# Kernel tuning notes

Hardware: AMD Instinct MI355X
Metric: run time of the kernel (lower is better)

Reference implementation:

```python
import jax, jax.numpy as jnp
import numpy as np

# Config matching init_kwargs
DILS = [1, 3, 6, 12]          # flattened dilations for blocks [[1,3],[6,12]]
BLOCK_START = [0, 2]          # layer index where each block starts
IN = 64                       # input_size
SS = 256                      # state_size
HS = 128                      # h_size
OS = SS - HS                  # out_size for S2Cell
OUT = 8                       # output_size
B = 1024                      # batch (number of series)
T = 256                       # timesteps
# per-layer lxh input widths: [in, out, out+in, out] each + 2*h
IN_SIZES = [IN + 2 * HS, OS + 2 * HS, OS + IN + 2 * HS, OS + 2 * HS]


def setup_inputs() -> dict:
    key = jax.random.key(0)
    ks = jax.random.split(key, 12)
    d = {"x": jax.random.normal(ks[0], (T, B, IN), jnp.float32)}
    for i in range(4):
        fan_in = IN_SIZES[i]
        d[f"W{i}"] = jax.random.normal(ks[1 + i], (4 * SS, fan_in), jnp.float32) / np.sqrt(fan_in)
        d[f"b{i}"] = jnp.zeros((4 * SS,), jnp.float32)
    d["Wout"] = jax.random.normal(ks[9], (OUT, OS), jnp.float32) / np.sqrt(OS)
    d["bout"] = jnp.zeros((OUT,), jnp.float32)
    return d


def _s2cell(t, inp, W, b, prevH, prevC, bufH, bufC, dil):
    """One S2Cell step. bufH/bufC are circular buffers of length dil holding
    states from the last `dil` steps; bufH[t % dil] is the state from t-dil."""
    idx = t % dil
    has_del = t >= dil
    dH = jnp.where(has_del, bufH[idx], prevH)   # [B, HS]
    dC = bufC[idx]                               # [B, SS] (only used when has_del)
    xh = jnp.concatenate([inp, prevH, dH], axis=1)
    gates = xh @ W.T + b                         # [B, 4*SS]
    g0, g1, g2, g3 = jnp.split(gates, 4, axis=1)
    forget = jax.nn.sigmoid(g0 + 1.0)
    cand = jnp.tanh(g1)
    alpha = jax.nn.sigmoid(g2)
    out_gate = jax.nn.sigmoid(g3)
    weightedC = jnp.where(has_del, alpha * prevC + (1.0 - alpha) * dC, prevC)
    newC = jnp.where(t >= 1, forget * weightedC + (1.0 - forget) * cand, cand)
    whole = out_gate * newC                      # [B, SS]
    out_t, h = whole[:, :OS], whole[:, OS:]
    return out_t, h, newC, bufH.at[idx].set(h), bufC.at[idx].set(newC)


def reference(x, W0, b0, W1, b1, W2, b2, W3, b3, Wout, bout):
    Ws = [W0, W1, W2, W3]
    bs = [b0, b1, b2, b3]

    def init_layer(d):
        return (jnp.zeros((B, HS), x.dtype), jnp.zeros((B, SS), x.dtype),
                jnp.zeros((d, B, HS), x.dtype), jnp.zeros((d, B, SS), x.dtype))

    carry0 = (jnp.int32(0), tuple(init_layer(d) for d in DILS))

    def step(carry, x_t):
        t, states = carry
        new_states = []
        inp = x_t
        for li in range(4):
            if li in BLOCK_START and li > 0:
                # first layer of a later block: cat(previous block output, original input)
                inp = jnp.concatenate([inp, x_t], axis=1)
            prevH, prevC, bufH, bufC = states[li]
            inp, h, c, bufH, bufC = _s2cell(t, inp, Ws[li], bs[li], prevH, prevC, bufH, bufC, DILS[li])
            new_states.append((h, c, bufH, bufC))
        y = inp @ Wout.T + bout
        return (t + 1, tuple(new_states)), y

    _, ys = jax.lax.scan(step, carry0, x)
    return ys  # [T, B, OUT]
```

## Files before the change

### kernel.cpp

```cpp
#include <hip/hip_runtime.h>
#include <stdint.h>
#include <stdio.h>


typedef __attribute__((ext_vector_type(8))) short short8;
typedef __attribute__((ext_vector_type(4))) float f32x4;

#define DEVINL static __device__ __forceinline__

constexpr int TT = 256, BBATCH = 1024, INW = 64, HSW = 128, OSW = 128, NO = 8;
constexpr int ROWS = 128;

constexpr int KLa[4]   = {192, 384, 448, 384};
constexpr int DILa[4]  = {1, 3, 6, 12};
constexpr int PERa[4]  = {2, 4, 7, 13};
constexpr int WOFFa[4] = {0, 6144, 18432, 32768};
constexpr int WBYTES   = 90112;

constexpr int BIAS_B  = WBYTES;
constexpr int WOUT_B  = BIAS_B + 512;
constexpr int WSTR    = 129;
constexpr int BOUT_B  = WOUT_B + 8 * WSTR * 4;
constexpr int C3_B    = BOUT_B + 32;
constexpr int LDS_BYTES = C3_B + 12 * 256 * 16;

constexpr size_t WSBASE    = 8192;
constexpr size_t BH_OFF[4] = {0, 65536, 196608, 425984};
constexpr size_t OUTB_OFF  = 851968;
constexpr size_t CB_OFF    = 983040;
constexpr size_t C1_SZ     = 32 * 3 * 256 * 16;
constexpr size_t C2_SZ     = 32 * 6 * 256 * 16;
constexpr size_t CLSZ      = CB_OFF + C1_SZ + C2_SZ;
constexpr size_t WS_NEED   = WSBASE + 8 * CLSZ;

__host__ __device__ constexpr int seg_type(int L, int k) {
  if (L == 0) return k < 64 ? 0 : 2;
  if (L == 1) return k < 128 ? 1 : (k < 256 ? 2 : 3);
  if (L == 2) return k < 128 ? 1 : (k < 192 ? 0 : (k < 320 ? 2 : 3));
  return k < 128 ? 1 : (k < 256 ? 2 : 3);
}
__host__ __device__ constexpr int seg_start(int L, int k) {
  if (L == 0) return k < 64 ? 0 : 64;
  if (L == 1) return k < 128 ? 0 : (k < 256 ? 128 : 256);
  if (L == 2) return k < 128 ? 0 : (k < 192 ? 128 : (k < 320 ? 192 : 320));
  return k < 128 ? 0 : (k < 256 ? 128 : 256);
}

template <int N> struct IC { static constexpr int value = N; };

DEVINL unsigned short f2bf(float f) {
  union { float f; uint32_t u; } v; v.f = f;
  return (unsigned short)((v.u + 0x7FFFu + ((v.u >> 16) & 1u)) >> 16);
}
DEVINL float bf2f(unsigned short h) {
  union { uint32_t u; float f; } v; v.u = ((uint32_t)h) << 16;
  return v.f;
}
DEVINL float sigm(float x)  { return 1.0f / (1.0f + __expf(-x)); }
DEVINL float tanh_(float x) { return 1.0f - 2.0f / (__expf(2.0f * x) + 1.0f); }

DEVINL short8 zero_s8() { short8 v; for (int i = 0; i < 8; i++) v[i] = 0; return v; }
DEVINL f32x4  zero_f4() { f32x4  v; for (int i = 0; i < 4; i++) v[i] = 0.f; return v; }

DEVINL f32x4 mfma16(short8 a, short8 b, f32x4 c) {
  return __builtin_amdgcn_mfma_f32_16x16x32_bf16(a, b, c, 0, 0, 0);
}

DEVINL short8 ld8f(const float* p) {
  const f32x4 u0 = *(const f32x4*)p;
  const f32x4 u1 = *(const f32x4*)(p + 4);
  short8 r;
  r[0] = (short)f2bf(u0[0]); r[1] = (short)f2bf(u0[1]);
  r[2] = (short)f2bf(u0[2]); r[3] = (short)f2bf(u0[3]);
  r[4] = (short)f2bf(u1[0]); r[5] = (short)f2bf(u1[1]);
  r[6] = (short)f2bf(u1[2]); r[7] = (short)f2bf(u1[3]);
  return r;
}

__global__ void __launch_bounds__(256, 1)
rnn_stack_kernel(const float* __restrict__ x,
                 const float* __restrict__ W0, const float* __restrict__ b0,
                 const float* __restrict__ W1, const float* __restrict__ b1,
                 const float* __restrict__ W2, const float* __restrict__ b2,
                 const float* __restrict__ W3, const float* __restrict__ b3,
                 const float* __restrict__ Wout, const float* __restrict__ bout,
                 float* __restrict__ yout, char* __restrict__ ws)
{
  extern __shared__ char smem[];
  unsigned short* wlds = (unsigned short*)smem;
  float* biasl = (float*)(smem + BIAS_B);
  float* woutl = (float*)(smem + WOUT_B);
  float* boutl = (float*)(smem + BOUT_B);
  float* c3l   = (float*)(smem + C3_B);

  const int tid = threadIdx.x;

  __shared__ unsigned s_cg;
  if (tid == 0) {
    unsigned xcc;
    asm volatile("s_getreg_b32 %0, hwreg(HW_REG_XCC_ID)" : "=s"(xcc));
    xcc &= 7u;
    unsigned rank = __hip_atomic_fetch_add(
        (unsigned*)(ws + 4096 + (size_t)xcc * 64), 1u,
        __ATOMIC_RELAXED, __HIP_MEMORY_SCOPE_AGENT);
    s_cg = (xcc << 8) | (rank & 31u);
  }
  __syncthreads();
  const int c = __builtin_amdgcn_readfirstlane((int)(s_cg >> 8));
  const int g = __builtin_amdgcn_readfirstlane((int)(s_cg & 255));

  char* cb = ws + WSBASE + (size_t)c * CLSZ;
  unsigned short* bufH[4];
  unsigned short* outb[4];
#pragma unroll
  for (int l = 0; l < 4; l++) {
    bufH[l] = (unsigned short*)(cb + BH_OFF[l]);
    outb[l] = (unsigned short*)(cb + OUTB_OFF + (size_t)l * ROWS * OSW * 2);
  }
  float* bufC1 = (float*)(cb + CB_OFF + (size_t)g * (3 * 256 * 16));
  float* bufC2 = (float*)(cb + CB_OFF + C1_SZ + (size_t)g * (6 * 256 * 16));

  {
    const float* Wsrc[4] = {W0, W1, W2, W3};
    const float* bsrc[4] = {b0, b1, b2, b3};
    for (int l = 0; l < 4; l++) {
      const int K = KLa[l];
      const int Ksrc = (l == 0) ? 320 : K;
      unsigned short* base = wlds + WOFFa[l];
      for (int n = 0; n < 32; n++) {
        const int grow = (n >> 3) * 256 + g * 8 + (n & 7);
        const float* src = Wsrc[l] + (size_t)grow * Ksrc;
        for (int k = tid; k < K; k += 256) {
          float v = src[k];
          if (l == 0 && k >= 64) v += src[k + 128];
          base[((k >> 5) * 2 + (n >> 4)) * 512 + (n & 15) * 32 +
               ((k >> 3) & 3) * 8 + (k & 7)] = f2bf(v);
        }
      }
      if (tid < 32) biasl[l * 32 + tid] = bsrc[l][(tid >> 3) * 256 + g * 8 + (tid & 7)];
    }
    for (int i = tid; i < 8 * 128; i += 256) woutl[(i >> 7) * WSTR + (i & 127)] = Wout[i];
    if (tid < 8) boutl[tid] = bout[tid];
  }
  __syncthreads();

  const int wv = tid >> 6, lane = tid & 63, lm = lane & 15, quad = lane >> 4;
  const int m0 = wv * 32;
  const bool hi = lm >= 8;
  const int j = lm & 7;
  const int mrow = m0 + (hi ? 16 : 0) + quad * 4;

  unsigned* flg = (unsigned*)(ws + (size_t)c * 512 + (size_t)wv * 128);

  f32x4 pc[4];
#pragma unroll
  for (int l = 0; l < 4; l++) pc[l] = zero_f4();

  f32x4 dc1 = zero_f4(), dc2 = zero_f4(), dc3 = zero_f4();

  auto arrive = [&](unsigned ep) {
    asm volatile("s_waitcnt vmcnt(0)" ::: "memory");
    if (lane == 0)
      __hip_atomic_store(flg + g, ep, __ATOMIC_RELAXED, __HIP_MEMORY_SCOPE_AGENT);
  };
  auto waitbar = [&](unsigned ep) {
    asm volatile("" ::: "memory");
    for (;;) {
      unsigned v = __hip_atomic_load(flg + (lane & 31), __ATOMIC_RELAXED,
                                     __HIP_MEMORY_SCOPE_AGENT);
      if (__all((int)(v >= ep))) break;
    }
    asm volatile("buffer_inv sc0" ::: "memory");
  };

  auto cellpub = [&](auto Lc, int t, f32x4& A00, f32x4& A01, f32x4& A10, f32x4& A11) {
    constexpr int L = decltype(Lc)::value;
    constexpr int DL = DILa[L];
    constexpr int P = PERa[L];
    f32x4 s00, s01, s10, s11;
#pragma unroll
    for (int r = 0; r < 4; r++) {
      s00[r] = __shfl_xor(A00[r], 8);
      s01[r] = __shfl_xor(A01[r], 8);
      s10[r] = __shfl_xor(A10[r], 8);
      s11[r] = __shfl_xor(A11[r], 8);
    }
    f32x4 G0, G1, G2, G3;
#pragma unroll
    for (int r = 0; r < 4; r++) {
      G0[r] = hi ? s10[r] : A00[r];
      G1[r] = hi ? A10[r] : s00[r];
      G2[r] = hi ? s11[r] : A01[r];
      G3[r] = hi ? A11[r] : s01[r];
    }
    const f32x4 pcv = pc[L];
    f32x4 dC = zero_f4();
    if constexpr (L == 1) dC = dc1;
    if constexpr (L == 2) dC = dc2;
    if constexpr (L == 3) dC = dc3;
    f32x4 nC, wh;
#pragma unroll
    for (int q = 0; q < 4; q++) {
      const float fg = sigm(G0[q]);
      const float cd = tanh_(G1[q]);
      const float og = sigm(G3[q]);
      float wc;
      if constexpr (L == 0) {
        wc = pcv[q];
      } else {
        const float al = sigm(G2[q]);
        wc = (t >= DL) ? (al * pcv[q] + (1.0f - al) * dC[q]) : pcv[q];
      }
      const float nc = (t >= 1) ? (fg * wc + (1.0f - fg) * cd) : cd;
      nC[q] = nc;
      wh[q] = og * nc;
    }
    if constexpr (L == 1) *(f32x4*)(bufC1 + ((size_t)(t % 3) * 256 + tid) * 4) = nC;
    if constexpr (L == 2) *(f32x4*)(bufC2 + ((size_t)(t % 6) * 256 + tid) * 4) = nC;
    if constexpr (L == 3) *(f32x4*)(c3l + ((size_t)(t % 12) * 256 + tid) * 4) = nC;
    pc[L] = nC;
    const int jg = g * 8 + j;
#pragma unroll
    for (int r = 0; r < 4; r++) {
      const unsigned short us = f2bf(wh[r]);
      const int row = mrow + r;
      if (g < 16) outb[L][(size_t)row * OSW + jg] = us;
      else bufH[L][((size_t)(t % P) * ROWS + row) * HSW + (jg - 128)] = us;
    }
  };

  auto preL = [&](auto Lc, int t, f32x4& A00, f32x4& A01, f32x4& A10, f32x4& A11) {
    constexpr int L = decltype(Lc)::value;
    constexpr int NKT = KLa[L] / 32;
    constexpr int DL = DILa[L];
    constexpr int P = PERa[L];
    const unsigned short* wl = wlds + WOFFa[L];
    const float bb0 = biasl[L * 32 + lm] + (lm < 8 ? 1.0f : 0.0f);
    const float bb1 = biasl[L * 32 + 16 + lm];
    A00 = (f32x4){bb0, bb0, bb0, bb0};
    A10 = A00;
    A01 = (f32x4){bb1, bb1, bb1, bb1};
    A11 = A01;
    const unsigned short* phb =
        (t >= 1) ? bufH[L] + (size_t)((t - 1) % P) * ROWS * HSW : nullptr;
    const unsigned short* dhb =
        (t >= DL) ? bufH[L] + (size_t)((t - DL) % P) * ROWS * HSW : phb;
    const float* xb = x + ((size_t)t * BBATCH + (size_t)c * ROWS) * INW;
#pragma unroll
    for (int kt = 0; kt < NKT; kt++) {
      const int sty = seg_type(L, kt * 32);
      if (sty == 1) continue;
      const int sst = seg_start(L, kt * 32);
      const int kloc = kt * 32 - sst + quad * 8;
      short8 a0, a1;
      if (sty == 0) {
        const float* p = xb + (size_t)(m0 + lm) * INW + kloc;
        a0 = ld8f(p);
        a1 = ld8f(p + 16 * INW);
      } else {
        const unsigned short* sb = (sty == 2) ? phb : dhb;
        if (sb) {
          const unsigned short* p = sb + (size_t)(m0 + lm) * HSW + kloc;
          a0 = *(const short8*)p;
          a1 = *(const short8*)(p + 16 * HSW);
        } else {
          a0 = zero_s8();
          a1 = zero_s8();
        }
      }
      const short8 bf0v = *(const short8*)(wl + (kt * 2 + 0) * 512 + lm * 32 + quad * 8);
      const short8 bf1v = *(const short8*)(wl + (kt * 2 + 1) * 512 + lm * 32 + quad * 8);
      A00 = mfma16(a0, bf0v, A00);
      A01 = mfma16(a0, bf1v, A01);
      A10 = mfma16(a1, bf0v, A10);
      A11 = mfma16(a1, bf1v, A11);
    }
  };

  auto postL = [&](auto Lc, int t, f32x4& A00, f32x4& A01, f32x4& A10, f32x4& A11) {
    constexpr int L = decltype(Lc)::value;
    const unsigned short* wl = wlds + WOFFa[L];
    const unsigned short* ob = outb[L - 1];
#pragma unroll
    for (int kt = 0; kt < 4; kt++) {
      const int kloc = kt * 32 + quad * 8;
      const unsigned short* p = ob + (size_t)(m0 + lm) * HSW + kloc;
      const short8 a0 = *(const short8*)p;
      const short8 a1 = *(const short8*)(p + 16 * HSW);
      const short8 bf0v = *(const short8*)(wl + (kt * 2 + 0) * 512 + lm * 32 + quad * 8);
      const short8 bf1v = *(const short8*)(wl + (kt * 2 + 1) * 512 + lm * 32 + quad * 8);
      A00 = mfma16(a0, bf0v, A00);
      A01 = mfma16(a0, bf1v, A01);
      A10 = mfma16(a1, bf0v, A10);
      A11 = mfma16(a1, bf1v, A11);
    }
    cellpub(Lc, t, A00, A01, A10, A11);
  };

  auto fullL0 = [&](int t) {
    if (t >= TT) return;
    f32x4 A00, A01, A10, A11;
    const unsigned short* wl = wlds + WOFFa[0];
    const float bb0 = biasl[lm] + (lm < 8 ? 1.0f : 0.0f);
    const float bb1 = biasl[16 + lm];
    A00 = (f32x4){bb0, bb0, bb0, bb0};
    A10 = A00;
    A01 = (f32x4){bb1, bb1, bb1, bb1};
    A11 = A01;
    const unsigned short* phb =
        (t >= 1) ? bufH[0] + (size_t)((t - 1) & 1) * ROWS * HSW : nullptr;
    const float* xb = x + ((size_t)t * BBATCH + (size_t)c * ROWS) * INW;
#pragma unroll
    for (int kt = 0; kt < 6; kt++) {
      const int sty = seg_type(0, kt * 32);
      const int sst = seg_start(0, kt * 32);
      const int kloc = kt * 32 - sst + quad * 8;
      short8 a0, a1;
      if (sty == 0) {
        const float* p = xb + (size_t)(m0 + lm) * INW + kloc;
        a0 = ld8f(p);
        a1 = ld8f(p + 16 * INW);
      } else if (phb) {
        const unsigned short* p = phb + (size_t)(m0 + lm) * HSW + kloc;
        a0 = *(const short8*)p;
        a1 = *(const short8*)(p + 16 * HSW);
      } else {
        a0 = zero_s8();
        a1 = zero_s8();
      }
      const short8 bf0v = *(const short8*)(wl + (kt * 2 + 0) * 512 + lm * 32 + quad * 8);
      const short8 bf1v = *(const short8*)(wl + (kt * 2 + 1) * 512 + lm * 32 + quad * 8);
      A00 = mfma16(a0, bf0v, A00);
      A01 = mfma16(a0, bf1v, A01);
      A10 = mfma16(a1, bf0v, A10);
      A11 = mfma16(a1, bf1v, A11);
    }
    cellpub(IC<0>{}, t, A00, A01, A10, A11);
  };

  auto touchx = [&](int t) {
    if (t >= TT) return;
    const float* xt = x + ((size_t)t * BBATCH + (size_t)c * ROWS + m0) * INW
                      + (size_t)lane * 32;
    float tmp;
    asm volatile("global_load_dword %0, %1, off"
                 : "=v"(tmp) : "v"(xt) : "memory");
  };

  auto epilogue = [&](int tt) {
    if (tt < 0) return;
    const int r = m0 + g;
    const unsigned short* orow = outb[3] + (size_t)r * OSW;
    const int o = lane >> 3, s = lane & 7;
    const short8 v0 = *(const short8*)(orow + s * 16);
    const short8 v1 = *(const short8*)(orow + s * 16 + 8);
    float part = 0.f;
#pragma unroll
    for (int i = 0; i < 8; i++)
      part += bf2f((unsigned short)v0[i]) * woutl[o * WSTR + s * 16 + i];
#pragma unroll
    for (int i = 0; i < 8; i++)
      part += bf2f((unsigned short)v1[i]) * woutl[o * WSTR + s * 16 + 8 + i];
    part += __shfl_down(part, 4);
    part += __shfl_down(part, 2);
    part += __shfl_down(part, 1);
    if (s == 0)
      yout[((size_t)tt * BBATCH + (size_t)c * ROWS + r) * NO + o] = part + boutl[o];
  };

  f32x4 a1_00, a1_01, a1_10, a1_11;
  f32x4 a2_00, a2_01, a2_10, a2_11;
  f32x4 a3_00, a3_01, a3_10, a3_11;

  fullL0(0);
  unsigned ep = 0;
  for (int t = 0; t < TT; t++) {
    if (t > 0) postL3_label: ;
    if (t > 0) postL(IC<3>{}, t - 1, a3_00, a3_01, a3_10, a3_11);
    arrive(++ep);
    preL(IC<1>{}, t, a1_00, a1_01, a1_10, a1_11);
    if (t >= 3) dc1 = *(const f32x4*)(bufC1 + ((size_t)(t % 3) * 256 + tid) * 4);
    waitbar(ep);
    postL(IC<1>{}, t, a1_00, a1_01, a1_10, a1_11);
    arrive(++ep);
    preL(IC<2>{}, t, a2_00, a2_01, a2_10, a2_11);
    if (t >= 6) dc2 = *(const f32x4*)(bufC2 + ((size_t)(t % 6) * 256 + tid) * 4);
    epilogue(t - 1);
    touchx(t + 2);
    waitbar(ep);
    postL(IC<2>{}, t, a2_00, a2_01, a2_10, a2_11);
    arrive(++ep);
    preL(IC<3>{}, t, a3_00, a3_01, a3_10, a3_11);
    if (t >= 12) dc3 = *(const f32x4*)(c3l + ((size_t)(t % 12) * 256 + tid) * 4);
    fullL0(t + 1);
    waitbar(ep);
  }
  postL(IC<3>{}, TT - 1, a3_00, a3_01, a3_10, a3_11);
  arrive(++ep);
  waitbar(ep);
  epilogue(TT - 1);
}

extern "C" void kernel_launch(void* const* d_in, const int* in_sizes, int n_in,
                              void* d_out, int out_size, void* d_ws, size_t ws_size,
                              hipStream_t stream) {
  const float* x    = (const float*)d_in[0];
  const float* W0   = (const float*)d_in[1];
  const float* b0   = (const float*)d_in[2];
  const float* W1   = (const float*)d_in[3];
  const float* b1   = (const float*)d_in[4];
  const float* W2   = (const float*)d_in[5];
  const float* b2   = (const float*)d_in[6];
  const float* W3   = (const float*)d_in[7];
  const float* b3   = (const float*)d_in[8];
  const float* Wout = (const float*)d_in[9];
  const float* bout = (const float*)d_in[10];
  float* out = (float*)d_out;
  char* ws = (char*)d_ws;

  if (ws_size < WS_NEED) {
    fprintf(stderr, "kernel_launch: ws_size %zu < needed %zu\n", ws_size, (size_t)WS_NEED);
    return;
  }

  hipMemsetAsync(d_ws, 0, 8192, stream);

  hipError_t e = hipFuncSetAttribute((const void*)rnn_stack_kernel,
                                     hipFuncAttributeMaxDynamicSharedMemorySize,
                                     LDS_BYTES);
  if (e != hipSuccess) fprintf(stderr, "hipFuncSetAttribute: %d\n", (int)e);

  rnn_stack_kernel<<<dim3(256), dim3(256), LDS_BYTES, stream>>>(
      x, W0, b0, W1, b1, W2, b2, W3, b3, Wout, bout, out, ws);
  e = hipGetLastError();
  if (e != hipSuccess) fprintf(stderr, "launch error: %d\n", (int)e);
}
```

Before: 4.387 ms.

## Prefetch x and post-barrier weight fragments into registers before each barrier wait

The x activations for layers 0 and 2 are now loaded and converted to bf16 into registers ahead of use, replacing the touch-only prefetch and the inline loads. The weight fragments for each layer's post-barrier K segment are read from LDS into registers before the spin wait, so the critical path after the barrier only reads the previous layer's output. A short s_sleep is added to the spin loop to reduce polling pressure. This raises register use and may add wake-up latency to the barrier.

Measured after the change: 4.972 ms. +13.3%, slower.

```diff
diff --git a/kernel.cpp b/kernel.cpp
--- a/kernel.cpp
+++ b/kernel.cpp
@@ -66,15 +66,16 @@
   return __builtin_amdgcn_mfma_f32_16x16x32_bf16(a, b, c, 0, 0, 0);
 }
 
+DEVINL short8 pk8(f32x4 a, f32x4 b) {
+  short8 r;
+  r[0] = (short)f2bf(a[0]); r[1] = (short)f2bf(a[1]);
+  r[2] = (short)f2bf(a[2]); r[3] = (short)f2bf(a[3]);
+  r[4] = (short)f2bf(b[0]); r[5] = (short)f2bf(b[1]);
+  r[6] = (short)f2bf(b[2]); r[7] = (short)f2bf(b[3]);
+  return r;
+}
 DEVINL short8 ld8f(const float* p) {
-  const f32x4 u0 = *(const f32x4*)p;
-  const f32x4 u1 = *(const f32x4*)(p + 4);
-  short8 r;
-  r[0] = (short)f2bf(u0[0]); r[1] = (short)f2bf(u0[1]);
-  r[2] = (short)f2bf(u0[2]); r[3] = (short)f2bf(u0[3]);
-  r[4] = (short)f2bf(u1[0]); r[5] = (short)f2bf(u1[1]);
-  r[6] = (short)f2bf(u1[2]); r[7] = (short)f2bf(u1[3]);
-  return r;
+  return pk8(*(const f32x4*)p, *(const f32x4*)(p + 4));
 }
 
 __global__ void __launch_bounds__(256, 1)
@@ -158,6 +159,10 @@
 
   f32x4 dc1 = zero_f4(), dc2 = zero_f4(), dc3 = zero_f4();
 
+  short8 wob[2][4];
+  short8 xa2[2][2];
+  short8 xa0[2][2];
+
   auto arrive = [&](unsigned ep) {
     asm volatile("s_waitcnt vmcnt(0)" ::: "memory");
     if (lane == 0)
@@ -169,8 +174,29 @@
       unsigned v = __hip_atomic_load(flg + (lane & 31), __ATOMIC_RELAXED,
                                      __HIP_MEMORY_SCOPE_AGENT);
       if (__all((int)(v >= ep))) break;
+      __builtin_amdgcn_s_sleep(1);
     }
     asm volatile("buffer_inv sc0" ::: "memory");
+  };
+
+  auto loadX = [&](short8 (&xa)[2][2], int t) {
+    if (t >= TT) return;
+    const float* xb = x + ((size_t)t * BBATCH + (size_t)c * ROWS) * INW;
+#pragma unroll
+    for (int kk = 0; kk < 2; kk++) {
+      const float* p = xb + (size_t)(m0 + lm) * INW + kk * 32 + quad * 8;
+      xa[0][kk] = ld8f(p);
+      xa[1][kk] = ld8f(p + 16 * INW);
+    }
+  };
+
+  auto loadWob = [&](int L) {
+    const unsigned short* wl = wlds + WOFFa[L];
+#pragma unroll
+    for (int kt = 0; kt < 4; kt++) {
+      wob[0][kt] = *(const short8*)(wl + (kt * 2 + 0) * 512 + lm * 32 + quad * 8);
+      wob[1][kt] = *(const short8*)(wl + (kt * 2 + 1) * 512 + lm * 32 + quad * 8);
+    }
   };
 
   auto cellpub = [&](auto Lc, int t, f32x4& A00, f32x4& A01, f32x4& A10, f32x4& A11) {
@@ -245,7 +271,6 @@
         (t >= 1) ? bufH[L] + (size_t)((t - 1) % P) * ROWS * HSW : nullptr;
     const unsigned short* dhb =
         (t >= DL) ? bufH[L] + (size_t)((t - DL) % P) * ROWS * HSW : phb;
-    const float* xb = x + ((size_t)t * BBATCH + (size_t)c * ROWS) * INW;
 #pragma unroll
     for (int kt = 0; kt < NKT; kt++) {
       const int sty = seg_type(L, kt * 32);
@@ -254,9 +279,13 @@
       const int kloc = kt * 32 - sst + quad * 8;
       short8 a0, a1;
       if (sty == 0) {
-        const float* p = xb + (size_t)(m0 + lm) * INW + kloc;
-        a0 = ld8f(p);
-        a1 = ld8f(p + 16 * INW);
+        if constexpr (L == 2) {
+          a0 = xa2[0][kt - 4];
+          a1 = xa2[1][kt - 4];
+        } else {
+          a0 = zero_s8();
+          a1 = zero_s8();
+        }
       } else {
         const unsigned short* sb = (sty == 2) ? phb : dhb;
         if (sb) {
@@ -279,7 +308,6 @@
 
   auto postL = [&](auto Lc, int t, f32x4& A00, f32x4& A01, f32x4& A10, f32x4& A11) {
     constexpr int L = decltype(Lc)::value;
-    const unsigned short* wl = wlds + WOFFa[L];
     const unsigned short* ob = outb[L - 1];
 #pragma unroll
     for (int kt = 0; kt < 4; kt++) {
@@ -287,12 +315,10 @@
       const unsigned short* p = ob + (size_t)(m0 + lm) * HSW + kloc;
       const short8 a0 = *(const short8*)p;
       const short8 a1 = *(const short8*)(p + 16 * HSW);
-      const short8 bf0v = *(const short8*)(wl + (kt * 2 + 0) * 512 + lm * 32 + quad * 8);
-      const short8 bf1v = *(const short8*)(wl + (kt * 2 + 1) * 512 + lm * 32 + quad * 8);
-      A00 = mfma16(a0, bf0v, A00);
-      A01 = mfma16(a0, bf1v, A01);
-      A10 = mfma16(a1, bf0v, A10);
-      A11 = mfma16(a1, bf1v, A11);
+      A00 = mfma16(a0, wob[0][kt], A00);
+      A01 = mfma16(a0, wob[1][kt], A01);
+      A10 = mfma16(a1, wob[0][kt], A10);
+      A11 = mfma16(a1, wob[1][kt], A11);
     }
     cellpub(Lc, t, A00, A01, A10, A11);
   };
@@ -309,7 +335,6 @@
     A11 = A01;
     const unsigned short* phb =
         (t >= 1) ? bufH[0] + (size_t)((t - 1) & 1) * ROWS * HSW : nullptr;
-    const float* xb = x + ((size_t)t * BBATCH + (size_t)c * ROWS) * INW;
 #pragma unroll
     for (int kt = 0; kt < 6; kt++) {
       const int sty = seg_type(0, kt * 32);
@@ -317,9 +342,8 @@
       const int kloc = kt * 32 - sst + quad * 8;
       short8 a0, a1;
       if (sty == 0) {
-        const float* p = xb + (size_t)(m0 + lm) * INW + kloc;
-        a0 = ld8f(p);
-        a1 = ld8f(p + 16 * INW);
+        a0 = xa0[0][kt];
+        a1 = xa0[1][kt];
       } else if (phb) {
         const unsigned short* p = phb + (size_t)(m0 + lm) * HSW + kloc;
         a0 = *(const short8*)p;
@@ -338,15 +362,6 @@
     cellpub(IC<0>{}, t, A00, A01, A10, A11);
   };
 
-  auto touchx = [&](int t) {
-    if (t >= TT) return;
-    const float* xt = x + ((size_t)t * BBATCH + (size_t)c * ROWS + m0) * INW
-                      + (size_t)lane * 32;
-    float tmp;
-    asm volatile("global_load_dword %0, %1, off"
-                 : "=v"(tmp) : "v"(xt) : "memory");
-  };
-
   auto epilogue = [&](int tt) {
     if (tt < 0) return;
     const int r = m0 + g;
@@ -372,27 +387,38 @@
   f32x4 a2_00, a2_01, a2_10, a2_11;
   f32x4 a3_00, a3_01, a3_10, a3_11;
 
+  loadX(xa0, 0);
   fullL0(0);
   unsigned ep = 0;
+
   for (int t = 0; t < TT; t++) {
-    if (t > 0) postL3_label: ;
     if (t > 0) postL(IC<3>{}, t - 1, a3_00, a3_01, a3_10, a3_11);
     arrive(++ep);
-    preL(IC<1>{}, t, a1_00, a1_01, a1_10, a1_11);
-    if (t >= 3) dc1 = *(const f32x4*)(bufC1 + ((size_t)(t % 3) * 256 + tid) * 4);
+    {
+      loadX(xa2, t);
+      preL(IC<1>{}, t, a1_00, a1_01, a1_10, a1_11);
+      if (t >= 3) dc1 = *(const f32x4*)(bufC1 + ((size_t)(t % 3) * 256 + tid) * 4);
+      loadWob(1);
+    }
     waitbar(ep);
     postL(IC<1>{}, t, a1_00, a1_01, a1_10, a1_11);
     arrive(++ep);
-    preL(IC<2>{}, t, a2_00, a2_01, a2_10, a2_11);
-    if (t >= 6) dc2 = *(const f32x4*)(bufC2 + ((size_t)(t % 6) * 256 + tid) * 4);
-    epilogue(t - 1);
-    touchx(t + 2);
+    {
+      loadX(xa0, t + 1);
+      preL(IC<2>{}, t, a2_00, a2_01, a2_10, a2_11);
+      if (t >= 6) dc2 = *(const f32x4*)(bufC2 + ((size_t)(t % 6) * 256 + tid) * 4);
+      epilogue(t - 1);
+      loadWob(2);
+    }
     waitbar(ep);
     postL(IC<2>{}, t, a2_00, a2_01, a2_10, a2_11);
     arrive(++ep);
-    preL(IC<3>{}, t, a3_00, a3_01, a3_10, a3_11);
-    if (t >= 12) dc3 = *(const f32x4*)(c3l + ((size_t)(t % 12) * 256 + tid) * 4);
-    fullL0(t + 1);
+    {
+      preL(IC<3>{}, t, a3_00, a3_01, a3_10, a3_11);
+      if (t >= 12) dc3 = *(const f32x4*)(c3l + ((size_t)(t % 12) * 256 + tid) * 4);
+      fullL0(t + 1);
+      loadWob(3);
+    }
     waitbar(ep);
   }
   postL(IC<3>{}, TT - 1, a3_00, a3_01, a3_10, a3_11);
```
